# Performance work log

Measured on AMD Instinct MI355X. Metric: run time of the kernel, lower is better.

Reference implementation:

```python
import jax, jax.numpy as jnp
import numpy as np

D_KEY, BANK_N = 128, 9720
BS, N = 1, 1620          # n = h*w = 30*54 (480p features, stride 16)
D_VAL, C, OBJ_N = 512, 512, 3


def setup_inputs() -> dict:
    key = jax.random.key(0)
    k1, k2, k3, k4, k5 = jax.random.split(key, 5)
    return {
        "keys_bank": jax.random.normal(k1, (D_KEY, BANK_N), dtype=jnp.float32),
        "q_in": jax.random.normal(k2, (BS, D_KEY, N), dtype=jnp.float32),
        "q_out": jax.random.normal(k3, (OBJ_N, C, N), dtype=jnp.float32),
        "values": jax.random.normal(k4, (OBJ_N, D_VAL, BANK_N), dtype=jnp.float32),
        "masks": jax.random.uniform(k5, (OBJ_N, 1, BANK_N), dtype=jnp.float32),
    }


def reference(keys_bank, q_in, q_out, values, masks):
    # p[b,k,n] = softmax_k( keys^T q_in / sqrt(d_key) )
    d_key = keys_bank.shape[0]
    scale = 1.0 / np.sqrt(d_key).astype(np.float32)
    p = jnp.einsum("dk,bdn->bkn", keys_bank, q_in) * scale
    p = jax.nn.softmax(p, axis=1)  # over bank dim

    # Batched over objects (original loops per object, sharing p)
    mem = jnp.einsum("ovk,bkn->obvn", values, p)       # (obj, bs, d_val, n)
    mask_mem = jnp.einsum("ouk,bkn->obun", masks, p)   # (obj, bs, 1, n)
    q_out_with_mask = q_out[:, None, :, :] * mask_mem  # (obj, bs, C, n)

    out = jnp.concatenate([mem, q_out_with_mask], axis=2)  # (obj, bs, d_val+C, n)
    return jnp.swapaxes(out, 0, 1)                          # (bs, obj, d_val+C, n)
```

## Files before the change

kernel.cpp:

```cpp
#include <hip/hip_runtime.h>
#include <hip/hip_bf16.h>

typedef unsigned short u16;
typedef unsigned char  u8;

#define D_KEY   128
#define BANK_N  9720
#define BANK_P  9728
#define N_TOK   1620
#define N_PAD   1664
#define OBJ_N   3
#define M_PAD   1664
#define LDCOL   1664
#define ONES_ROW 1539
#define QK_SCALE 0.08838834764831845f
#define KITERS  76

typedef __bf16 bf16x8 __attribute__((ext_vector_type(8)));
typedef float  f32x4  __attribute__((ext_vector_type(4)));
typedef unsigned int u32x4 __attribute__((ext_vector_type(4)));
typedef int i32x8 __attribute__((ext_vector_type(8)));

__device__ __forceinline__ float bf2f(u16 u) {
  union { unsigned int i; float f; } v; v.i = ((unsigned int)u) << 16; return v.f;
}
__device__ __forceinline__ u16 f2bf(float f) {
  unsigned int x = __float_as_uint(f);
  unsigned int r = x + 0x7fffu + ((x >> 16) & 1u);
  return (u16)(r >> 16);
}
__device__ __forceinline__ unsigned pack_fp8x4(float a, float b, float c, float d) {
  unsigned v = __builtin_amdgcn_cvt_pk_fp8_f32(a, b, 0, false);
  v = __builtin_amdgcn_cvt_pk_fp8_f32(c, d, v, true);
  return v;
}
__device__ __forceinline__ u8 f2fp8(float a) {
  return (u8)(__builtin_amdgcn_cvt_pk_fp8_f32(a, 0.f, 0, false) & 0xff);
}

__device__ __forceinline__ void load_lds16(const void* g, void* l) {
  __builtin_amdgcn_global_load_lds(
      (const __attribute__((address_space(1))) void*)g,
      (__attribute__((address_space(3))) void*)l, 16, 0, 0);
}

__global__ void prep(const float* __restrict__ q, const float* __restrict__ keys,
                     const float* __restrict__ values, const float* __restrict__ masks,
                     u16* __restrict__ qT, u16* __restrict__ kT, u8* __restrict__ vm8) {
  __shared__ float t[64][65];
  int b = blockIdx.x;
  const int tx = threadIdx.x & 63;
  const int ty = threadIdx.x >> 6;
  if (b < 52) {
    const int bd = (b & 1) * 64;
    const int bn = (b >> 1) * 64;
#pragma unroll
    for (int i = 0; i < 64; i += 4) {
      int d = bd + ty + i;
      int n = bn + tx;
      t[ty + i][tx] = (n < N_TOK) ? q[(size_t)d * N_TOK + n] : 0.f;
    }
    __syncthreads();
#pragma unroll
    for (int i = 0; i < 64; i += 4) {
      int r = ty + i;
      qT[(size_t)(bn + r) * D_KEY + bd + tx] = f2bf(t[tx][r] * QK_SCALE);
    }
    return;
  }
  if (b < 356) {
    b -= 52;
    const int bk = (b % 152) * 64;
    const int bd = (b / 152) * 64;
#pragma unroll
    for (int i = 0; i < 64; i += 4) {
      int d = bd + ty + i;
      int k = bk + tx;
      t[ty + i][tx] = (k < BANK_N) ? keys[(size_t)d * BANK_N + k] : 0.f;
    }
    __syncthreads();
#pragma unroll
    for (int i = 0; i < 64; i += 4) {
      int r = ty + i;
      kT[(size_t)(bk + r) * D_KEY + bd + tx] = f2bf(t[tx][r]);
    }
    return;
  }
  const int NV = BANK_P / 16;
  int idx = (b - 356) * 256 + threadIdx.x;
  if (idx >= M_PAD * NV) return;
  int m = idx / NV;
  int k16 = (idx - m * NV) * 16;
  const bool ones = (m == ONES_ROW);
  const float* src = nullptr;
  if (m < 1536)          src = values + (size_t)m * BANK_N;
  else if (m < ONES_ROW) src = masks + (size_t)(m - 1536) * BANK_N;
  u32x4 outv;
#pragma unroll
  for (int c = 0; c < 4; c++) {
    int k4 = k16 + c * 4;
    float4 v = make_float4(0.f, 0.f, 0.f, 0.f);
    if (ones) {
      v.x = (k4     < BANK_N) ? 1.f : 0.f;
      v.y = (k4 + 1 < BANK_N) ? 1.f : 0.f;
      v.z = (k4 + 2 < BANK_N) ? 1.f : 0.f;
      v.w = (k4 + 3 < BANK_N) ? 1.f : 0.f;
    } else if (src) {
      if (k4 + 3 < BANK_N) v = *(const float4*)(src + k4);
      else {
        if (k4     < BANK_N) v.x = src[k4];
        if (k4 + 1 < BANK_N) v.y = src[k4 + 1];
        if (k4 + 2 < BANK_N) v.z = src[k4 + 2];
        if (k4 + 3 < BANK_N) v.w = src[k4 + 3];
      }
    }
    outv[c] = pack_fp8x4(v.x, v.y, v.z, v.w);
  }
  *(u32x4*)(vm8 + (size_t)m * BANK_P + k16) = outv;
}

__global__ void gemm_qk(const u16* __restrict__ A, const u16* __restrict__ B,
                        u8* __restrict__ E8)
{
  __shared__ __align__(16) u16 sbuf[8192];
  u16* As = sbuf;
  u16* Bs = sbuf + 4096;

  const int tid  = threadIdx.x;
  const int wave = tid >> 6;
  const int lane = tid & 63;
  const int bn = blockIdx.x % 76, bm = blockIdx.x / 76;

  const u16* Abase = A + (size_t)bm * 128 * D_KEY;
  const u16* Bbase = B + (size_t)bn * 128 * D_KEY;

  const int r  = lane >> 2;
  const int c8 = (lane & 3) << 3;
  const int s0 = wave, s1 = wave + 4;

  f32x4 acc[4][4];
#pragma unroll
  for (int i = 0; i < 4; i++)
#pragma unroll
    for (int j = 0; j < 4; j++) acc[i][j] = (f32x4){0.f, 0.f, 0.f, 0.f};

  const int m_in = lane & 15;
  const int quad = lane >> 4;
  const int wm = (wave >> 1) * 64;
  const int wn = (wave & 1) * 64;

  for (int kt = 0; kt < D_KEY; kt += 32) {
    load_lds16(Abase + (size_t)(s0 * 16 + r) * D_KEY + kt + c8, &As[s0 * 512]);
    load_lds16(Abase + (size_t)(s1 * 16 + r) * D_KEY + kt + c8, &As[s1 * 512]);
    load_lds16(Bbase + (size_t)(s0 * 16 + r) * D_KEY + kt + c8, &Bs[s0 * 512]);
    load_lds16(Bbase + (size_t)(s1 * 16 + r) * D_KEY + kt + c8, &Bs[s1 * 512]);
    __syncthreads();

    bf16x8 af[4], bfr[4];
#pragma unroll
    for (int i = 0; i < 4; i++)
      af[i] = *(const bf16x8*)&As[(wm + i * 16 + m_in) * 32 + quad * 8];
#pragma unroll
    for (int j = 0; j < 4; j++)
      bfr[j] = *(const bf16x8*)&Bs[(wn + j * 16 + m_in) * 32 + quad * 8];
#pragma unroll
    for (int i = 0; i < 4; i++)
#pragma unroll
      for (int j = 0; j < 4; j++)
        acc[i][j] = __builtin_amdgcn_mfma_f32_16x16x32_bf16(af[i], bfr[j], acc[i][j], 0, 0, 0);
    __syncthreads();
  }

  u8* sb8 = (u8*)sbuf;
#pragma unroll
  for (int i = 0; i < 4; i++)
#pragma unroll
    for (int j = 0; j < 4; j++)
#pragma unroll
      for (int t = 0; t < 4; t++) {
        int row_l = wm + i * 16 + quad * 4 + t;
        int col_l = wn + j * 16 + m_in;
        bool valid = (bn * 128 + col_l) < BANK_N;
        sb8[(row_l << 7) + col_l] = valid ? f2fp8(__expf(acc[i][j][t])) : (u8)0;
      }
  __syncthreads();

  for (int chunk = tid; chunk < 1024; chunk += 256) {
    int row = chunk >> 3;
    int cu  = (chunk & 7) << 4;
    u32x4 v = *(const u32x4*)&sb8[(row << 7) + cu];
    *(u32x4*)&E8[(size_t)(bm * 128 + row) * BANK_P + bn * 128 + cu] = v;
  }
}

__global__ __launch_bounds__(256, 3)
void gemm_pv(const u8* __restrict__ A, const u8* __restrict__ B,
             u16* __restrict__ memC, int nParts, size_t cPartStride)
{
  __shared__ __align__(16) u16 sbuf[16384];
  u8* As8 = (u8*)sbuf;
  u8* Bs8 = (u8*)sbuf + 16384;

  const int tid  = threadIdx.x;
  const int wave = tid >> 6;
  const int lane = tid & 63;

  const int bq = (int)gridDim.x >> 3, br = (int)gridDim.x & 7;
  const int xcd = blockIdx.x & 7, bj = blockIdx.x >> 3;
  int b = (xcd < br ? xcd * (bq + 1) : br * (bq + 1) + (xcd - br) * bq) + bj;

  int bz = b / 169;
  int rr = b - bz * 169;
  int gid = rr / 52;
  int rem = rr - gid * 52;
  int width = (gid < 3) ? 4 : 1;
  int bm = rem / width;
  int bn = gid * 4 + (rem - bm * width);

  const int base = KITERS / nParts;
  const int remP = KITERS - base * nParts;
  const int nt    = base + (bz < remP ? 1 : 0);
  const int itbeg = bz * base + (bz < remP ? bz : remP);
  const int kbeg  = itbeg * 128;

  const u8* Abase = A + (size_t)bm * 128 * BANK_P;
  const u8* Bbase = B + (size_t)bn * 128 * BANK_P;

  const int srow  = lane >> 1;
  const int shalf = (((lane & 1) ^ ((lane >> 3) & 1)) << 4);

  f32x4 acc[4][4];
#pragma unroll
  for (int i = 0; i < 4; i++)
#pragma unroll
    for (int j = 0; j < 4; j++) acc[i][j] = (f32x4){0.f, 0.f, 0.f, 0.f};

  const int m_in = lane & 15;
  const int quad = lane >> 4;
  const int wm = (wave >> 1) * 64;
  const int wn = (wave & 1) * 64;
  const int fxor = ((m_in >> 2) & 1) << 4;

  const size_t arow_off = (size_t)(wave * 32 + srow) * BANK_P;

  for (int it = 0; it < nt; ++it) {
    const int kt = kbeg + it * 128;
#pragma unroll
    for (int s = 0; s < 4; s++)
      load_lds16(Abase + arow_off + kt + s * 32 + shalf, As8 + s * 4096 + wave * 1024);
#pragma unroll
    for (int s = 0; s < 4; s++)
      load_lds16(Bbase + arow_off + kt + s * 32 + shalf, Bs8 + s * 4096 + wave * 1024);
    __syncthreads();

    i32x8 a8[4];
#pragma unroll
    for (int i = 0; i < 4; i++) {
      const u8* p = As8 + quad * 4096 + (wm + i * 16 + m_in) * 32;
      u32x4 lo = *(const u32x4*)(p + fxor);
      u32x4 hi = *(const u32x4*)(p + (fxor ^ 16));
      a8[i] = (i32x8){(int)lo[0], (int)lo[1], (int)lo[2], (int)lo[3],
                      (int)hi[0], (int)hi[1], (int)hi[2], (int)hi[3]};
    }
#pragma unroll
    for (int j = 0; j < 4; j++) {
      const u8* p = Bs8 + quad * 4096 + (wn + j * 16 + m_in) * 32;
      u32x4 lo = *(const u32x4*)(p + fxor);
      u32x4 hi = *(const u32x4*)(p + (fxor ^ 16));
      i32x8 b8 = (i32x8){(int)lo[0], (int)lo[1], (int)lo[2], (int)lo[3],
                         (int)hi[0], (int)hi[1], (int)hi[2], (int)hi[3]};
#pragma unroll
      for (int i = 0; i < 4; i++)
        acc[i][j] = __builtin_amdgcn_mfma_scale_f32_16x16x128_f8f6f4(
            a8[i], b8, acc[i][j], 0, 0,
            0, 0x7f7f7f7f, 0, 0x7f7f7f7f);
    }
    __syncthreads();
  }

  u16* Cg = memC + (size_t)bz * cPartStride;
#pragma unroll
  for (int h = 0; h < 2; h++) {
    __syncthreads();
    if ((wave >> 1) == h) {
#pragma unroll
      for (int i = 0; i < 4; i++)
#pragma unroll
        for (int j = 0; j < 4; j++)
#pragma unroll
          for (int t = 0; t < 4; t++) {
            int row_l = i * 16 + quad * 4 + t;
            int col_l = wn + j * 16 + m_in;
            sbuf[(row_l << 7) + col_l] = f2bf(acc[i][j][t]);
          }
    }
    __syncthreads();
    for (int chunk = tid; chunk < 1024; chunk += 256) {
      int row = chunk >> 4;
      int cu  = (chunk & 15) << 3;
      u32x4 v = *(const u32x4*)&sbuf[(row << 7) + cu];
      __builtin_nontemporal_store(
          v, (u32x4*)&Cg[(size_t)(bm * 128 + h * 64 + row) * LDCOL + bn * 128 + cu]);
    }
  }
}

__global__ void lsum_inv_k(const u16* __restrict__ memC, float* __restrict__ inv_l,
                           int nParts) {
  int n = blockIdx.x * 256 + threadIdx.x;
  if (n >= N_TOK) return;
  const size_t ps = (size_t)M_PAD * LDCOL;
  const u16* p = memC + (size_t)ONES_ROW * LDCOL + n;
  float s = 0.f;
  for (int z = 0; z < nParts; z++) s += bf2f(p[(size_t)z * ps]);
  inv_l[n] = 1.f / s;
}

__global__ void epilogue(const u16* __restrict__ memC, const float* __restrict__ q_out,
                         const float* __restrict__ inv_l, float* __restrict__ out,
                         int nParts) {
  const int NV = N_TOK / 4;
  int idx = blockIdx.x * 256 + threadIdx.x;
  if (idx >= OBJ_N * 1024 * NV) return;
  int n4 = (idx % NV) * 4;
  int t = idx / NV;
  int c = t & 1023;
  int o = t >> 10;
  const size_t ps = (size_t)M_PAD * LDCOL;

  float4 il = *(const float4*)(inv_l + n4);

  size_t rowoff = (c < 512) ? (size_t)(o * 512 + c) * LDCOL
                            : (size_t)(1536 + o) * LDCOL;
  const u16* base = memC + rowoff + n4;
  float4 s = make_float4(0.f, 0.f, 0.f, 0.f);
  for (int z = 0; z < nParts; z++) {
    ushort4 v = *(const ushort4*)(base + z * ps);
    s.x += bf2f(v.x); s.y += bf2f(v.y); s.z += bf2f(v.z); s.w += bf2f(v.w);
  }
  float4 rv;
  if (c < 512) {
    rv.x = s.x * il.x; rv.y = s.y * il.y; rv.z = s.z * il.z; rv.w = s.w * il.w;
  } else {
    float4 q = *(const float4*)(q_out + (size_t)(o * 512 + (c - 512)) * N_TOK + n4);
    rv.x = q.x * s.x * il.x; rv.y = q.y * s.y * il.y;
    rv.z = q.z * s.z * il.z; rv.w = q.w * s.w * il.w;
  }
  *(float4*)(out + (size_t)(o * 1024 + c) * N_TOK + n4) = rv;
}

extern "C" void kernel_launch(void* const* d_in, const int* in_sizes, int n_in,
                              void* d_out, int out_size, void* d_ws, size_t ws_size,
                              hipStream_t stream) {
  const float* keys   = (const float*)d_in[0];
  const float* q_in   = (const float*)d_in[1];
  const float* q_out  = (const float*)d_in[2];
  const float* values = (const float*)d_in[3];
  const float* masks  = (const float*)d_in[4];
  float* out = (float*)d_out;

  char* ws = (char*)d_ws;
  size_t off = 0;
  auto alloc = [&](size_t bytes) -> void* {
    void* p = ws + off; off += (bytes + 255) & ~(size_t)255; return p;
  };
  u16*  qT    = (u16*)alloc((size_t)N_PAD * D_KEY * 2);
  u16*  kT    = (u16*)alloc((size_t)BANK_P * D_KEY * 2);
  u8*   vm8   = (u8*)alloc((size_t)M_PAD * BANK_P);
  u8*   E8    = (u8*)alloc((size_t)N_PAD * BANK_P);
  float* inv_l = (float*)alloc((size_t)N_PAD * 4);

  int nParts = 8;
  while (nParts > 1 && off + (size_t)nParts * M_PAD * LDCOL * 2 > ws_size) nParts >>= 1;
  u16* memC = (u16*)alloc((size_t)nParts * M_PAD * LDCOL * 2);

  const int vmBlocks = (M_PAD * (BANK_P / 16) + 255) / 256;
  prep<<<356 + vmBlocks, 256, 0, stream>>>(q_in, keys, values, masks, qT, kT, vm8);

  gemm_qk<<<988, 256, 0, stream>>>(qT, kT, E8);

  gemm_pv<<<dim3(169 * nParts), 256, 0, stream>>>(vm8, E8, memC, nParts, (size_t)M_PAD * LDCOL);

  lsum_inv_k<<<(N_TOK + 255) / 256, 256, 0, stream>>>(memC, inv_l, nParts);

  epilogue<<<(OBJ_N * 1024 * (N_TOK / 4) + 255) / 256, 256, 0, stream>>>(
      memC, q_out, inv_l, out, nParts);
}
```

Baseline: 198.0 us.

## Overlap value fp8 conversion with QK GEMM and fold row-sum into epilogue

```diff
diff --git a/kernel.cpp b/kernel.cpp
--- a/kernel.cpp
+++ b/kernel.cpp
@@ -15,6 +15,7 @@
 #define ONES_ROW 1539
 #define QK_SCALE 0.08838834764831845f
 #define KITERS  76
+#define QK_BLOCKS 988
 
 typedef __bf16 bf16x8 __attribute__((ext_vector_type(8)));
 typedef float  f32x4  __attribute__((ext_vector_type(4)));
@@ -45,8 +46,7 @@
 }
 
 __global__ void prep(const float* __restrict__ q, const float* __restrict__ keys,
-                     const float* __restrict__ values, const float* __restrict__ masks,
-                     u16* __restrict__ qT, u16* __restrict__ kT, u8* __restrict__ vm8) {
+                     u16* __restrict__ qT, u16* __restrict__ kT) {
   __shared__ float t[64][65];
   int b = blockIdx.x;
   const int tx = threadIdx.x & 63;
@@ -68,61 +68,66 @@
     }
     return;
   }
-  if (b < 356) {
-    b -= 52;
-    const int bk = (b % 152) * 64;
-    const int bd = (b / 152) * 64;
-#pragma unroll
-    for (int i = 0; i < 64; i += 4) {
-      int d = bd + ty + i;
-      int k = bk + tx;
-      t[ty + i][tx] = (k < BANK_N) ? keys[(size_t)d * BANK_N + k] : 0.f;
-    }
-    __syncthreads();
-#pragma unroll
-    for (int i = 0; i < 64; i += 4) {
-      int r = ty + i;
-      kT[(size_t)(bk + r) * D_KEY + bd + tx] = f2bf(t[tx][r]);
-    }
-    return;
-  }
-  const int NV = BANK_P / 16;
-  int idx = (b - 356) * 256 + threadIdx.x;
-  if (idx >= M_PAD * NV) return;
-  int m = idx / NV;
-  int k16 = (idx - m * NV) * 16;
-  const bool ones = (m == ONES_ROW);
-  const float* src = nullptr;
-  if (m < 1536)          src = values + (size_t)m * BANK_N;
-  else if (m < ONES_ROW) src = masks + (size_t)(m - 1536) * BANK_N;
-  u32x4 outv;
-#pragma unroll
-  for (int c = 0; c < 4; c++) {
-    int k4 = k16 + c * 4;
-    float4 v = make_float4(0.f, 0.f, 0.f, 0.f);
-    if (ones) {
-      v.x = (k4     < BANK_N) ? 1.f : 0.f;
-      v.y = (k4 + 1 < BANK_N) ? 1.f : 0.f;
-      v.z = (k4 + 2 < BANK_N) ? 1.f : 0.f;
-      v.w = (k4 + 3 < BANK_N) ? 1.f : 0.f;
-    } else if (src) {
-      if (k4 + 3 < BANK_N) v = *(const float4*)(src + k4);
-      else {
-        if (k4     < BANK_N) v.x = src[k4];
-        if (k4 + 1 < BANK_N) v.y = src[k4 + 1];
-        if (k4 + 2 < BANK_N) v.z = src[k4 + 2];
-        if (k4 + 3 < BANK_N) v.w = src[k4 + 3];
-      }
-    }
-    outv[c] = pack_fp8x4(v.x, v.y, v.z, v.w);
-  }
-  *(u32x4*)(vm8 + (size_t)m * BANK_P + k16) = outv;
-}
-
-__global__ void gemm_qk(const u16* __restrict__ A, const u16* __restrict__ B,
-                        u8* __restrict__ E8)
+  b -= 52;
+  const int bk = (b % 152) * 64;
+  const int bd = (b / 152) * 64;
+#pragma unroll
+  for (int i = 0; i < 64; i += 4) {
+    int d = bd + ty + i;
+    int k = bk + tx;
+    t[ty + i][tx] = (k < BANK_N) ? keys[(size_t)d * BANK_N + k] : 0.f;
+  }
+  __syncthreads();
+#pragma unroll
+  for (int i = 0; i < 64; i += 4) {
+    int r = ty + i;
+    kT[(size_t)(bk + r) * D_KEY + bd + tx] = f2bf(t[tx][r]);
+  }
+}
+
+__global__ void gemm_qk_vm(const u16* __restrict__ A, const u16* __restrict__ B,
+                           u8* __restrict__ E8,
+                           const float* __restrict__ values,
+                           const float* __restrict__ masks,
+                           u8* __restrict__ vm8)
 {
   __shared__ __align__(16) u16 sbuf[8192];
+
+  if (blockIdx.x >= QK_BLOCKS) {
+    const int NV = BANK_P / 16;
+    int idx = (blockIdx.x - QK_BLOCKS) * 256 + threadIdx.x;
+    if (idx >= M_PAD * NV) return;
+    int m = idx / NV;
+    int k16 = (idx - m * NV) * 16;
+    const bool ones = (m == ONES_ROW);
+    const float* src = nullptr;
+    if (m < 1536)          src = values + (size_t)m * BANK_N;
+    else if (m < ONES_ROW) src = masks + (size_t)(m - 1536) * BANK_N;
+    u32x4 outv;
+#pragma unroll
+    for (int c = 0; c < 4; c++) {
+      int k4 = k16 + c * 4;
+      float4 v = make_float4(0.f, 0.f, 0.f, 0.f);
+      if (ones) {
+        v.x = (k4     < BANK_N) ? 1.f : 0.f;
+        v.y = (k4 + 1 < BANK_N) ? 1.f : 0.f;
+        v.z = (k4 + 2 < BANK_N) ? 1.f : 0.f;
+        v.w = (k4 + 3 < BANK_N) ? 1.f : 0.f;
+      } else if (src) {
+        if (k4 + 3 < BANK_N) v = *(const float4*)(src + k4);
+        else {
+          if (k4     < BANK_N) v.x = src[k4];
+          if (k4 + 1 < BANK_N) v.y = src[k4 + 1];
+          if (k4 + 2 < BANK_N) v.z = src[k4 + 2];
+          if (k4 + 3 < BANK_N) v.w = src[k4 + 3];
+        }
+      }
+      outv[c] = pack_fp8x4(v.x, v.y, v.z, v.w);
+    }
+    *(u32x4*)(vm8 + (size_t)m * BANK_P + k16) = outv;
+    return;
+  }
+
   u16* As = sbuf;
   u16* Bs = sbuf + 4096;
 
@@ -305,20 +310,8 @@
   }
 }
 
-__global__ void lsum_inv_k(const u16* __restrict__ memC, float* __restrict__ inv_l,
-                           int nParts) {
-  int n = blockIdx.x * 256 + threadIdx.x;
-  if (n >= N_TOK) return;
-  const size_t ps = (size_t)M_PAD * LDCOL;
-  const u16* p = memC + (size_t)ONES_ROW * LDCOL + n;
-  float s = 0.f;
-  for (int z = 0; z < nParts; z++) s += bf2f(p[(size_t)z * ps]);
-  inv_l[n] = 1.f / s;
-}
-
 __global__ void epilogue(const u16* __restrict__ memC, const float* __restrict__ q_out,
-                         const float* __restrict__ inv_l, float* __restrict__ out,
-                         int nParts) {
+                         float* __restrict__ out, int nParts) {
   const int NV = N_TOK / 4;
   int idx = blockIdx.x * 256 + threadIdx.x;
   if (idx >= OBJ_N * 1024 * NV) return;
@@ -328,7 +321,12 @@
   int o = t >> 10;
   const size_t ps = (size_t)M_PAD * LDCOL;
 
-  float4 il = *(const float4*)(inv_l + n4);
+  const u16* lbase = memC + (size_t)ONES_ROW * LDCOL + n4;
+  float4 l = make_float4(0.f, 0.f, 0.f, 0.f);
+  for (int z = 0; z < nParts; z++) {
+    ushort4 v = *(const ushort4*)(lbase + z * ps);
+    l.x += bf2f(v.x); l.y += bf2f(v.y); l.z += bf2f(v.z); l.w += bf2f(v.w);
+  }
 
   size_t rowoff = (c < 512) ? (size_t)(o * 512 + c) * LDCOL
                             : (size_t)(1536 + o) * LDCOL;
@@ -339,12 +337,13 @@
     s.x += bf2f(v.x); s.y += bf2f(v.y); s.z += bf2f(v.z); s.w += bf2f(v.w);
   }
   float4 rv;
+  float ix = 1.f / l.x, iy = 1.f / l.y, iz = 1.f / l.z, iw = 1.f / l.w;
   if (c < 512) {
-    rv.x = s.x * il.x; rv.y = s.y * il.y; rv.z = s.z * il.z; rv.w = s.w * il.w;
+    rv.x = s.x * ix; rv.y = s.y * iy; rv.z = s.z * iz; rv.w = s.w * iw;
   } else {
     float4 q = *(const float4*)(q_out + (size_t)(o * 512 + (c - 512)) * N_TOK + n4);
-    rv.x = q.x * s.x * il.x; rv.y = q.y * s.y * il.y;
-    rv.z = q.z * s.z * il.z; rv.w = q.w * s.w * il.w;
+    rv.x = q.x * s.x * ix; rv.y = q.y * s.y * iy;
+    rv.z = q.z * s.z * iz; rv.w = q.w * s.w * iw;
   }
   *(float4*)(out + (size_t)(o * 1024 + c) * N_TOK + n4) = rv;
 }
@@ -364,25 +363,22 @@
   auto alloc = [&](size_t bytes) -> void* {
     void* p = ws + off; off += (bytes + 255) & ~(size_t)255; return p;
   };
-  u16*  qT    = (u16*)alloc((size_t)N_PAD * D_KEY * 2);
-  u16*  kT    = (u16*)alloc((size_t)BANK_P * D_KEY * 2);
-  u8*   vm8   = (u8*)alloc((size_t)M_PAD * BANK_P);
-  u8*   E8    = (u8*)alloc((size_t)N_PAD * BANK_P);
-  float* inv_l = (float*)alloc((size_t)N_PAD * 4);
+  u16* qT  = (u16*)alloc((size_t)N_PAD * D_KEY * 2);
+  u16* kT  = (u16*)alloc((size_t)BANK_P * D_KEY * 2);
+  u8*  vm8 = (u8*)alloc((size_t)M_PAD * BANK_P);
+  u8*  E8  = (u8*)alloc((size_t)N_PAD * BANK_P);
 
   int nParts = 8;
   while (nParts > 1 && off + (size_t)nParts * M_PAD * LDCOL * 2 > ws_size) nParts >>= 1;
   u16* memC = (u16*)alloc((size_t)nParts * M_PAD * LDCOL * 2);
 
+  prep<<<356, 256, 0, stream>>>(q_in, keys, qT, kT);
+
   const int vmBlocks = (M_PAD * (BANK_P / 16) + 255) / 256;
-  prep<<<356 + vmBlocks, 256, 0, stream>>>(q_in, keys, values, masks, qT, kT, vm8);
-
-  gemm_qk<<<988, 256, 0, stream>>>(qT, kT, E8);
+  gemm_qk_vm<<<QK_BLOCKS + vmBlocks, 256, 0, stream>>>(qT, kT, E8, values, masks, vm8);
 
   gemm_pv<<<dim3(169 * nParts), 256, 0, stream>>>(vm8, E8, memC, nParts, (size_t)M_PAD * LDCOL);
 
-  lsum_inv_k<<<(N_TOK + 255) / 256, 256, 0, stream>>>(memC, inv_l, nParts);
-
   epilogue<<<(OBJ_N * 1024 * (N_TOK / 4) + 255) / 256, 256, 0, stream>>>(
-      memC, q_out, inv_l, out, nParts);
-}
+      memC, q_out, out, nParts);
+}
```

Result: no change. 197.1 us (-0.5%).
